# Optimization experiments

Hardware: AMD Instinct MI355X
Metric: run time of the kernel (lower is better)

Reference implementation:

```python
import jax, jax.numpy as jnp
import numpy as np

EPS = 1e-5
N_HEAD = 8

def setup_inputs() -> dict:
    key = jax.random.key(0)
    ks = jax.random.split(key, 8)
    n, c, h, w = 8, 512, 64, 64
    feats_in = 512
    x = jax.random.normal(ks[0], (n, c, h, w), jnp.float32)
    cond = jax.random.normal(ks[1], (n, feats_in), jnp.float32)
    # AdaGN linear: feats_in -> 2*c
    W_ada = jax.random.normal(ks[2], (feats_in, 2 * c), jnp.float32) * (1.0 / np.sqrt(feats_in))
    b_ada = jnp.zeros((2 * c,), jnp.float32)
    # qkv 1x1 conv: c -> 3c
    W_qkv = jax.random.normal(ks[3], (3 * c, c), jnp.float32) * (1.0 / np.sqrt(c))
    b_qkv = jnp.zeros((3 * c,), jnp.float32)
    # out 1x1 conv: c -> c
    W_out = jax.random.normal(ks[4], (c, c), jnp.float32) * (1.0 / np.sqrt(c))
    b_out = jnp.zeros((c,), jnp.float32)
    return {"x": x, "cond": cond, "W_ada": W_ada, "b_ada": b_ada,
            "W_qkv": W_qkv, "b_qkv": b_qkv, "W_out": W_out, "b_out": b_out}

def reference(x, cond, W_ada, b_ada, W_qkv, b_qkv, W_out, b_out):
    n, c, h, w = x.shape
    nh = N_HEAD
    dh = c // nh
    s = h * w
    # AdaGN: GroupNorm with 1 group, no affine, then scale/shift from cond
    scales_shifts = cond @ W_ada + b_ada  # [n, 2c]
    scales, shifts = scales_shifts[:, :c], scales_shifts[:, c:]
    xf = x.reshape(n, -1)
    mean = xf.mean(axis=1, keepdims=True)
    var = xf.var(axis=1, keepdims=True)
    normed = ((xf - mean) * jax.lax.rsqrt(var + EPS)).reshape(n, c, h, w)
    normed = shifts[:, :, None, None] + normed * (scales[:, :, None, None] + 1.0)
    # qkv 1x1 conv
    qkv = jnp.einsum('nchw,oc->nohw', normed, W_qkv) + b_qkv[None, :, None, None]
    # view [n, nh*3, dh, s] then transpose -> [n, nh*3, s, dh]
    qkv = qkv.reshape(n, nh * 3, dh, s).transpose(0, 1, 3, 2)
    q, k, v = jnp.split(qkv, 3, axis=1)  # each [n, nh, s, dh]
    scale = dh ** (-0.25)
    att = jnp.einsum('nhsd,nhtd->nhst', q * scale, k * scale)
    att = jax.nn.softmax(att, axis=-1)
    y = jnp.einsum('nhst,nhtd->nhsd', att, v)  # [n, nh, s, dh]
    y = y.transpose(0, 1, 3, 2).reshape(n, c, h, w)
    out = jnp.einsum('nchw,oc->nohw', y, W_out) + b_out[None, :, None, None]
    return x + out
```

## Files before the change

### kernel.cpp

```cpp
#include <hip/hip_runtime.h>

#define NB   8
#define CC   512
#define SS   4096
#define NHD  8
#define DH   64
#define FEAT 512
#define NPER (CC*SS)

typedef unsigned short ushort_t;
typedef __attribute__((ext_vector_type(8))) short bf16x8;
typedef __attribute__((ext_vector_type(4))) float f32x4;

__device__ inline float b2f(ushort_t h) {
    union { unsigned int u; float f; } v; v.u = ((unsigned int)h) << 16; return v.f;
}
__device__ inline ushort_t f2b(float f) {
    union { float f; unsigned int u; } v; v.f = f;
    unsigned int u = v.u;
    u += 0x7fffu + ((u >> 16) & 1u);
    return (ushort_t)(u >> 16);
}
__device__ inline void unpack8(uint4 v, ushort_t* us) {
    us[0] = v.x & 0xffff; us[1] = v.x >> 16;
    us[2] = v.y & 0xffff; us[3] = v.y >> 16;
    us[4] = v.z & 0xffff; us[5] = v.z >> 16;
    us[6] = v.w & 0xffff; us[7] = v.w >> 16;
}
__device__ inline float loadIn(const void* p, size_t idx, int isf) {
    return isf ? ((const float*)p)[idx] : b2f(((const ushort_t*)p)[idx]);
}
__device__ inline void load8(const void* p, size_t idx, int isf, float* f) {
    if (isf) {
        const float* q = (const float*)p + idx;
        float4 a = *(const float4*)q, b = *(const float4*)(q + 4);
        f[0]=a.x; f[1]=a.y; f[2]=a.z; f[3]=a.w; f[4]=b.x; f[5]=b.y; f[6]=b.z; f[7]=b.w;
    } else {
        uint4 v = *(const uint4*)((const ushort_t*)p + idx);
        ushort_t us[8]; unpack8(v, us);
        for (int j = 0; j < 8; ++j) f[j] = b2f(us[j]);
    }
}

typedef __attribute__((address_space(1))) const unsigned int gas_u32;
typedef __attribute__((address_space(3))) unsigned int las_u32;
__device__ inline void gload_lds16(const void* g, void* l) {
    __builtin_amdgcn_global_load_lds((gas_u32*)g, (las_u32*)l, 16, 0, 0);
}

__global__ void probe_kernel(const unsigned int* __restrict__ x, int* __restrict__ flag) {
    unsigned int w = x[threadIdx.x & 63];
    unsigned int elo = (w >> 7) & 0xFF;
    int hit = (elo >= 0x60 && elo <= 0x9F) ? 1 : 0;
    for (int m = 1; m < 64; m <<= 1) hit += __shfl_xor(hit, m, 64);
    if (threadIdx.x == 0) *flag = (hit >= 40) ? 0 : 1;
}

__global__ __launch_bounds__(256) void ada_kernel(
    const void* __restrict__ cond, const void* __restrict__ W,
    const void* __restrict__ bias, float* __restrict__ out,
    const int* __restrict__ flagp)
{
    int isf = *flagp;
    int n = blockIdx.x;
    int j = blockIdx.y * 256 + threadIdx.x;
    float acc = loadIn(bias, j, isf);
    for (int k = 0; k < FEAT; ++k)
        acc += loadIn(cond, (size_t)n * FEAT + k, isf) * loadIn(W, (size_t)k * (2 * CC) + j, isf);
    out[n * (2 * CC) + j] = acc;
}

__global__ __launch_bounds__(256) void stats_kernel(
    const void* __restrict__ x, float* __restrict__ part, const int* __restrict__ flagp)
{
    int isf = *flagp;
    int n = blockIdx.x, blk = blockIdx.y;
    int tid = threadIdx.x;
    float s = 0.f, ss = 0.f;
    size_t base8 = (size_t)blk * 4096 + tid;
    for (int i = 0; i < 16; ++i) {
        float f[8];
        load8(x, ((size_t)n * NPER) + (base8 + (size_t)i * 256) * 8, isf, f);
        for (int j = 0; j < 8; ++j) { s += f[j]; ss += f[j] * f[j]; }
    }
    for (int m = 1; m < 64; m <<= 1) { s += __shfl_xor(s, m, 64); ss += __shfl_xor(ss, m, 64); }
    int w = tid >> 6;
    if ((tid & 63) == 0) {
        part[(size_t)n * 512 + (blk * 4 + w) * 2 + 0] = s;
        part[(size_t)n * 512 + (blk * 4 + w) * 2 + 1] = ss;
    }
}

__global__ __launch_bounds__(256) void coef_kernel(
    const float* __restrict__ ada, const float* __restrict__ part,
    float* __restrict__ coefA, float* __restrict__ coefB)
{
    __shared__ float reds[4], redss[4], mv[2];
    int n = blockIdx.x;
    int tid = threadIdx.x;
    float s  = part[(size_t)n * 512 + tid * 2 + 0];
    float ss = part[(size_t)n * 512 + tid * 2 + 1];
    for (int m = 1; m < 64; m <<= 1) { s += __shfl_xor(s, m, 64); ss += __shfl_xor(ss, m, 64); }
    int w = tid >> 6, lane = tid & 63;
    if (lane == 0) { reds[w] = s; redss[w] = ss; }
    __syncthreads();
    if (tid == 0) {
        float S  = (reds[0] + reds[1]) + (reds[2] + reds[3]);
        float S2 = (redss[0] + redss[1]) + (redss[2] + redss[3]);
        float inv = 1.f / (float)NPER;
        float mean = S * inv;
        float var  = S2 * inv - mean * mean;
        mv[0] = mean;
        mv[1] = rsqrtf(var + 1e-5f);
    }
    __syncthreads();
    float mean = mv[0], r = mv[1];
    int c = blockIdx.y * 256 + tid;
    float a = (ada[n * (2 * CC) + c] + 1.f) * r;
    coefA[n * CC + c] = a;
    coefB[n * CC + c] = ada[n * (2 * CC) + CC + c] - mean * a;
}

__global__ __launch_bounds__(256) void wprime_kernel(
    const void* __restrict__ W, const void* __restrict__ bias,
    const float* __restrict__ coefA, const float* __restrict__ coefB,
    ushort_t* __restrict__ Wp, float* __restrict__ bias2,
    const int* __restrict__ flagp)
{
    int isf = *flagp;
    int n = blockIdx.x;
    int o = blockIdx.y * 256 + threadIdx.x;
    const float* cA = coefA + n * CC;
    const float* cB = coefB + n * CC;
    float bacc = loadIn(bias, o, isf);
    ushort_t* dst = Wp + ((size_t)n * 1536 + o) * 512;
    for (int c = 0; c < 512; c += 8) {
        float wv[8];
        load8(W, (size_t)o * 512 + c, isf, wv);
        float4 a0 = *(const float4*)&cA[c], a1 = *(const float4*)&cA[c + 4];
        float4 b0 = *(const float4*)&cB[c], b1 = *(const float4*)&cB[c + 4];
        float av[8] = {a0.x, a0.y, a0.z, a0.w, a1.x, a1.y, a1.z, a1.w};
        float bv[8] = {b0.x, b0.y, b0.z, b0.w, b1.x, b1.y, b1.z, b1.w};
        ushort_t pk[8];
        for (int j = 0; j < 8; ++j) {
            bacc += wv[j] * bv[j];
            pk[j] = f2b(wv[j] * av[j]);
        }
        *(ushort4*)&dst[c]     = make_ushort4(pk[0], pk[1], pk[2], pk[3]);
        *(ushort4*)&dst[c + 4] = make_ushort4(pk[4], pk[5], pk[6], pk[7]);
    }
    bias2[n * 1536 + o] = bacc;
}

__global__ __launch_bounds__(256) void wconv_kernel(
    const void* __restrict__ W, ushort_t* __restrict__ Wb, const int* __restrict__ flagp)
{
    int isf = *flagp;
    size_t i = ((size_t)blockIdx.x * 256 + threadIdx.x) * 8;
    float f[8];
    load8(W, i, isf, f);
    ushort_t pk[8];
    for (int j = 0; j < 8; ++j) pk[j] = f2b(f[j]);
    *(ushort4*)&Wb[i]     = make_ushort4(pk[0], pk[1], pk[2], pk[3]);
    *(ushort4*)&Wb[i + 4] = make_ushort4(pk[4], pk[5], pk[6], pk[7]);
}

__global__ __launch_bounds__(256) void xt_kernel(
    const void* __restrict__ x, ushort_t* __restrict__ xt, const int* __restrict__ flagp)
{
    __shared__ __align__(16) short xl[64][72];
    int isf = *flagp;
    int st = blockIdx.x & 63, ct = blockIdx.x >> 6;
    int n = blockIdx.y;
    int s0 = st * 64, c0 = ct * 64;
    int tid = threadIdx.x;
    for (int it = 0; it < 2; ++it) {
        int t = tid + it * 256;
        int cr = t >> 3, sc8 = t & 7;
        float f[8];
        load8(x, ((size_t)n * CC + c0 + cr) * SS + s0 + sc8 * 8, isf, f);
        ushort_t pk[8];
        for (int j = 0; j < 8; ++j) pk[j] = f2b(f[j]);
        *(ushort4*)&xl[cr][sc8 * 8]     = make_ushort4(pk[0], pk[1], pk[2], pk[3]);
        *(ushort4*)&xl[cr][sc8 * 8 + 4] = make_ushort4(pk[4], pk[5], pk[6], pk[7]);
    }
    __syncthreads();
    for (int it = 0; it < 2; ++it) {
        int t = tid + it * 256;
        int sr = t >> 3, cc8 = t & 7;
        ushort_t pk[8];
        for (int j = 0; j < 8; ++j) pk[j] = (ushort_t)xl[cc8 * 8 + j][sr];
        size_t o = ((size_t)n * SS + s0 + sr) * CC + c0 + cc8 * 8;
        *(ushort4*)&xt[o]     = make_ushort4(pk[0], pk[1], pk[2], pk[3]);
        *(ushort4*)&xt[o + 4] = make_ushort4(pk[4], pk[5], pk[6], pk[7]);
    }
}

__global__ __launch_bounds__(256) void qkv_gemm_kernel(
    const ushort_t* __restrict__ Wp, const ushort_t* __restrict__ xt,
    const float* __restrict__ bias2, ushort_t* __restrict__ C,
    int nb, int hb, int hc)
{
    __shared__ __align__(16) short Alds[3][64][64];
    __shared__ __align__(16) short Blds[64][64];
    int z = blockIdx.x;
    int nIdx = nb + z;
    int n0 = blockIdx.y * 64;
    int hh = blockIdx.z;
    int head = hb + hh;
    int hcc = hc * 64;
    int tid = threadIdx.x;
    int w = tid >> 6, lane = tid & 63;
    int quad = lane >> 4, l16 = lane & 15;
    int wm = (w >> 1) * 32, wn = (w & 1) * 32;
    const ushort_t* Ab = Wp + ((size_t)nIdx * 1536 + head * 64) * 512;
    const ushort_t* Bb = xt + ((size_t)nIdx * SS + n0) * 512;
    f32x4 acc[3][2][2] = {};

    int chunk0 = tid, chunk1 = tid + 256;
    int row0 = chunk0 >> 3, ssl0 = (chunk0 & 7) ^ (row0 & 7);
    int row1 = chunk1 >> 3, ssl1 = (chunk1 & 7) ^ (row1 & 7);
    int cb0a = w * 64, cb0b = 256 + w * 64;

    for (int k0 = 0; k0 < 512; k0 += 64) {
        __syncthreads();
        gload_lds16(&Bb[(size_t)row0 * 512 + k0 + ssl0 * 8], (short*)Blds + cb0a * 8);
        gload_lds16(&Bb[(size_t)row1 * 512 + k0 + ssl1 * 8], (short*)Blds + cb0b * 8);
        #pragma unroll
        for (int p = 0; p < 3; ++p) {
            const ushort_t* Ap = Ab + (size_t)p * 512 * 512;
            gload_lds16(&Ap[(size_t)row0 * 512 + k0 + ssl0 * 8], (short*)Alds[p] + cb0a * 8);
            gload_lds16(&Ap[(size_t)row1 * 512 + k0 + ssl1 * 8], (short*)Alds[p] + cb0b * 8);
        }
        __syncthreads();
        for (int kk = 0; kk < 2; ++kk) {
            bf16x8 bfv[2];
            for (int ni = 0; ni < 2; ++ni)
                bfv[ni] = *(const bf16x8*)&Blds[wn + ni * 16 + l16]
                                               [((kk * 4 + quad) ^ (l16 & 7)) * 8];
            #pragma unroll
            for (int p = 0; p < 3; ++p) {
                bf16x8 af[2];
                for (int mi = 0; mi < 2; ++mi)
                    af[mi] = *(const bf16x8*)&Alds[p][wm + mi * 16 + l16]
                                                     [((kk * 4 + quad) ^ (l16 & 7)) * 8];
                for (int mi = 0; mi < 2; ++mi)
                    for (int ni = 0; ni < 2; ++ni)
                        acc[p][mi][ni] = __builtin_amdgcn_mfma_f32_16x16x32_bf16(
                            af[mi], bfv[ni], acc[p][mi][ni], 0, 0, 0);
            }
        }
    }

    const float* b2p = bias2 + (size_t)nIdx * 1536;
    #pragma unroll
    for (int p = 0; p < 3; ++p) {
        int arow0 = p * 512 + head * 64;
        size_t cbase = ((size_t)(z * 3 + p) * hcc + hh * 64) * SS;
        if (p < 2) {
            const float SCL = 0.42467078f;
            for (int mi = 0; mi < 2; ++mi)
                for (int ni = 0; ni < 2; ++ni) {
                    int col = n0 + wn + ni * 16 + l16;
                    int d0 = wm + mi * 16 + quad * 4;
                    ushort_t pk[4];
                    for (int r = 0; r < 4; ++r) {
                        float v = (acc[p][mi][ni][r] + b2p[arow0 + d0 + r]) * SCL;
                        pk[r] = f2b(v);
                    }
                    *(ushort4*)&C[cbase + (size_t)col * 64 + d0] =
                        make_ushort4(pk[0], pk[1], pk[2], pk[3]);
                }
        } else {
            for (int mi = 0; mi < 2; ++mi)
                for (int ni = 0; ni < 2; ++ni) {
                    int col = n0 + wn + ni * 16 + l16;
                    for (int r = 0; r < 4; ++r) {
                        int rowl = wm + mi * 16 + quad * 4 + r;
                        float v = acc[p][mi][ni][r] + b2p[arow0 + rowl];
                        C[cbase + (size_t)rowl * SS + col] = f2b(v);
                    }
                }
        }
    }
}

__global__ __launch_bounds__(256, 4) void attn_kernel(
    const ushort_t* __restrict__ qkv,
    ushort_t* __restrict__ y,
    int nb, int hb, int hc)
{
    __shared__ __align__(16) short Klds[2][64][64];
    __shared__ __align__(16) short Vlds[2][64][64];

    int s0 = blockIdx.x * 128;
    int hl = blockIdx.y;
    int z = blockIdx.z;
    int n = nb + z;
    int hcc = hc * 64;
    const ushort_t* Q = qkv + ((size_t)(z * 3 + 0) * hcc + hl * 64) * SS;
    const ushort_t* K = qkv + ((size_t)(z * 3 + 1) * hcc + hl * 64) * SS;
    const ushort_t* V = qkv + ((size_t)(z * 3 + 2) * hcc + hl * 64) * SS;

    int tid = threadIdx.x;
    int w = tid >> 6, lane = tid & 63;
    int quad = lane >> 4, l16 = lane & 15;
    int sw = l16 & 7;

    bf16x8 qf[2][2];
    for (int si = 0; si < 2; ++si)
        for (int kk = 0; kk < 2; ++kk)
            qf[si][kk] = *(const bf16x8*)&Q[(size_t)(s0 + w * 32 + si * 16 + l16) * 64
                                            + kk * 32 + quad * 8];

    auto stage = [&](int b, int tt) {
        #pragma unroll
        for (int it = 0; it < 2; ++it) {
            int chunk = it * 256 + tid;
            int row = chunk >> 3;
            int ssl = (chunk & 7) ^ (row & 7);
            int cb0 = it * 256 + w * 64;
            gload_lds16(&K[(size_t)(tt + row) * 64 + ssl * 8], (short*)Klds[b] + cb0 * 8);
            gload_lds16(&V[(size_t)row * SS + tt + ssl * 8],   (short*)Vlds[b] + cb0 * 8);
        }
    };

    const short ONE = 0x3F80;
    bf16x8 ones = { ONE, ONE, ONE, ONE, ONE, ONE, ONE, ONE };

    f32x4 o[2][4] = {};
    f32x4 sum_acc[2] = {};

    stage(0, 0);

    for (int t0 = 0; t0 < SS; t0 += 64) {
        int cur = (t0 >> 6) & 1;
        __syncthreads();
        if (t0 + 64 < SS) stage(cur ^ 1, t0 + 64);

        for (int kk = 0; kk < 2; ++kk) {
            f32x4 sv[2][2];
            for (int ntl = 0; ntl < 2; ++ntl) {
                int nt = kk * 2 + ntl;
                bf16x8 kf0 = *(const bf16x8*)&Klds[cur][nt * 16 + l16][((0 * 4 + quad) ^ sw) * 8];
                bf16x8 kf1 = *(const bf16x8*)&Klds[cur][nt * 16 + l16][((1 * 4 + quad) ^ sw) * 8];
                for (int si = 0; si < 2; ++si) {
                    f32x4 a = { -16.f, -16.f, -16.f, -16.f };
                    a = __builtin_amdgcn_mfma_f32_16x16x32_bf16(kf0, qf[si][0], a, 0, 0, 0);
                    a = __builtin_amdgcn_mfma_f32_16x16x32_bf16(kf1, qf[si][1], a, 0, 0, 0);
                    sv[ntl][si] = a;
                }
            }

            bf16x8 vf[4];
            for (int dt = 0; dt < 4; ++dt)
                vf[dt] = *(const bf16x8*)&Vlds[cur][dt * 16 + l16][((kk * 4 + quad) ^ sw) * 8];

            for (int si = 0; si < 2; ++si) {
                float p0 = exp2f(sv[0][si][0]), p1 = exp2f(sv[0][si][1]);
                float p2 = exp2f(sv[0][si][2]), p3 = exp2f(sv[0][si][3]);
                float p4 = exp2f(sv[1][si][0]), p5 = exp2f(sv[1][si][1]);
                float p6 = exp2f(sv[1][si][2]), p7 = exp2f(sv[1][si][3]);
                unsigned int x0, x1, y0, y1;
                asm("v_cvt_pk_bf16_f32 %0, %1, %2" : "=v"(x0) : "v"(p0), "v"(p1));
                asm("v_cvt_pk_bf16_f32 %0, %1, %2" : "=v"(x1) : "v"(p2), "v"(p3));
                asm("v_cvt_pk_bf16_f32 %0, %1, %2" : "=v"(y0) : "v"(p4), "v"(p5));
                asm("v_cvt_pk_bf16_f32 %0, %1, %2" : "=v"(y1) : "v"(p6), "v"(p7));
                asm("v_permlane32_swap_b32 %0, %1" : "+v"(x0), "+v"(y0));
                asm("v_permlane32_swap_b32 %0, %1" : "+v"(x1), "+v"(y1));
                asm("v_permlane16_swap_b32 %0, %1" : "+v"(x0), "+v"(y0));
                asm("v_permlane16_swap_b32 %0, %1" : "+v"(x1), "+v"(y1));
                union { unsigned int u[4]; bf16x8 v; } frag;
                frag.u[0] = x0; frag.u[1] = x1; frag.u[2] = y0; frag.u[3] = y1;

                sum_acc[si] = __builtin_amdgcn_mfma_f32_16x16x32_bf16(frag.v, ones, sum_acc[si], 0, 0, 0);
                for (int dt = 0; dt < 4; ++dt)
                    o[si][dt] = __builtin_amdgcn_mfma_f32_16x16x32_bf16(frag.v, vf[dt], o[si][dt], 0, 0, 0);
            }
        }
    }

    for (int si = 0; si < 2; ++si) {
        f32x4 inv;
        for (int r = 0; r < 4; ++r) inv[r] = 1.0f / sum_acc[si][r];
        for (int dt = 0; dt < 4; ++dt) {
            int d = dt * 16 + l16;
            int cidx = (hb + hl) * DH + d;
            size_t bidx = ((size_t)n * CC + cidx) * SS + s0 + w * 32 + si * 16 + quad * 4;
            ushort_t pk[4];
            for (int r = 0; r < 4; ++r) pk[r] = f2b(o[si][dt][r] * inv[r]);
            *(ushort4*)&y[bidx] = make_ushort4(pk[0], pk[1], pk[2], pk[3]);
        }
    }
}

__global__ __launch_bounds__(512) void out_gemm_kernel(
    const ushort_t* __restrict__ Wb, const void* __restrict__ bias, const void* __restrict__ x,
    const ushort_t* __restrict__ ybuf, float* __restrict__ out,
    const int* __restrict__ flagp)
{
    __shared__ __align__(16) short Ylds[64][264];
    int isf = *flagp;
    int n = blockIdx.y;
    int s0 = blockIdx.x * 64;
    int tid = threadIdx.x;
    int w = tid >> 6, lane = tid & 63;
    int quad = lane >> 4, l16 = lane & 15;
    const ushort_t* Yb = ybuf + (size_t)n * ((size_t)CC * SS);
    float* Op = out + (size_t)n * NPER;

    f32x4 acc[4][4] = {};
    for (int kh = 0; kh < 2; ++kh) {
        __syncthreads();
        int ch = (tid & 255) + kh * 256;
        int cg = tid >> 8;
        for (int cb = 0; cb < 4; ++cb) {
            uint4 v = *(const uint4*)&Yb[(size_t)ch * SS + s0 + cg * 32 + cb * 8];
            ushort_t us[8]; unpack8(v, us);
            for (int j = 0; j < 8; ++j) Ylds[cg * 32 + cb * 8 + j][tid & 255] = (short)us[j];
        }
        __syncthreads();
        for (int k0 = 0; k0 < 256; k0 += 32) {
            bf16x8 af[4];
            for (int mi = 0; mi < 4; ++mi)
                af[mi] = *(const bf16x8*)&Wb[(size_t)(w * 64 + mi * 16 + l16) * 512
                                             + kh * 256 + k0 + quad * 8];
            for (int ni = 0; ni < 4; ++ni) {
                bf16x8 bfv = *(const bf16x8*)&Ylds[ni * 16 + l16][k0 + quad * 8];
                for (int mi = 0; mi < 4; ++mi)
                    acc[mi][ni] = __builtin_amdgcn_mfma_f32_16x16x32_bf16(
                        af[mi], bfv, acc[mi][ni], 0, 0, 0);
            }
        }
    }

    for (int mi = 0; mi < 4; ++mi)
        for (int ni = 0; ni < 4; ++ni) {
            int col = s0 + ni * 16 + l16;
            for (int r = 0; r < 4; ++r) {
                int m = w * 64 + mi * 16 + quad * 4 + r;
                size_t idx = (size_t)m * SS + col;
                float v = acc[mi][ni][r] + loadIn(bias, m, isf)
                        + loadIn(x, (size_t)n * NPER + idx, isf);
                Op[idx] = v;
            }
        }
}

extern "C" void kernel_launch(void* const* d_in, const int* in_sizes, int n_in,
                              void* d_out, int out_size, void* d_ws, size_t ws_size,
                              hipStream_t stream) {
    (void)in_sizes; (void)n_in; (void)out_size;
    const void* x     = d_in[0];
    const void* cond  = d_in[1];
    const void* W_ada = d_in[2];
    const void* b_ada = d_in[3];
    const void* W_qkv = d_in[4];
    const void* b_qkv = d_in[5];
    const void* W_out = d_in[6];
    const void* b_out = d_in[7];
    float* out = (float*)d_out;

    char* ws = (char*)d_ws;
    float* part   = (float*)ws;
    float* ada    = (float*)(ws + 16384);
    float* coefA  = (float*)(ws + 49152);
    float* coefB  = (float*)(ws + 65536);
    int*   flag   = (int*)(ws + 81920);
    ushort_t* woutb  = (ushort_t*)(ws + 82176);
    float* bias2  = (float*)(ws + 606464);
    ushort_t* wprime = (ushort_t*)(ws + 655616);
    ushort_t* ybuf   = (ushort_t*)(ws + 13238528);
    ushort_t* xtb    = (ushort_t*)(ws + 46792960);
    const size_t BASE = 46792960ULL + 33554432ULL;
    ushort_t* qkvbuf = (ushort_t*)(ws + BASE);

    const size_t PER_HS = (size_t)3 * 64 * SS * 2;
    size_t avail = ws_size > BASE ? ws_size - BASE : 0;
    int NC = 1, HC = 1;
    if      (avail >= 64 * PER_HS) { NC = 8; HC = 8; }
    else if (avail >= 32 * PER_HS) { NC = 4; HC = 8; }
    else if (avail >= 16 * PER_HS) { NC = 2; HC = 8; }
    else if (avail >=  8 * PER_HS) { NC = 1; HC = 8; }
    else if (avail >=  4 * PER_HS) { NC = 1; HC = 4; }
    else if (avail >=  2 * PER_HS) { NC = 1; HC = 2; }

    probe_kernel <<<1, 64, 0, stream>>>((const unsigned int*)x, flag);
    ada_kernel   <<<dim3(NB, 4),  256, 0, stream>>>(cond, W_ada, b_ada, ada, flag);
    stats_kernel <<<dim3(NB, 64), 256, 0, stream>>>(x, part, flag);
    coef_kernel  <<<dim3(NB, 2),  256, 0, stream>>>(ada, part, coefA, coefB);
    wprime_kernel<<<dim3(NB, 6),  256, 0, stream>>>(W_qkv, b_qkv, coefA, coefB, wprime, bias2, flag);
    wconv_kernel <<<dim3(128),    256, 0, stream>>>(W_out, woutb, flag);
    xt_kernel    <<<dim3(512, NB), 256, 0, stream>>>(x, xtb, flag);

    for (int nb = 0; nb < NB; nb += NC)
        for (int hb = 0; hb < NHD; hb += HC) {
            qkv_gemm_kernel<<<dim3(NC, 64, HC), 256, 0, stream>>>(
                wprime, xtb, bias2, qkvbuf, nb, hb, HC);
            attn_kernel<<<dim3(32, HC, NC), 256, 0, stream>>>(
                qkvbuf, ybuf, nb, hb, HC);
        }

    out_gemm_kernel<<<dim3(64, NB), 512, 0, stream>>>(woutb, b_out, x, ybuf, out, flag);
}
```

Measured before the change: 841.4 us.

## Store attention output token-major and read it directly in output GEMM

The attention kernel now writes its output as [n, s, c] (token-major) rather than channel-major, so the output projection GEMM can load B fragments straight from global memory with contiguous 16-byte reads. This removes the LDS transpose staging, its scalar shared-memory stores and two barriers per K half in the output GEMM. In exchange, the attention epilogue does scattered 2-byte stores with a stride of CC elements, which may hurt write coalescing. The GEMM also now relies on global/L2 reuse of Y across the 8 waves instead of shared memory.

```diff
diff --git a/kernel.cpp b/kernel.cpp
--- a/kernel.cpp
+++ b/kernel.cpp
@@ -287,7 +287,7 @@
 
 __global__ __launch_bounds__(256, 4) void attn_kernel(
     const ushort_t* __restrict__ qkv,
-    ushort_t* __restrict__ y,
+    ushort_t* __restrict__ yt,
     int nb, int hb, int hc)
 {
     __shared__ __align__(16) short Klds[2][64][64];
@@ -380,58 +380,45 @@
         }
     }
 
+    int c0 = (hb + hl) * DH;
     for (int si = 0; si < 2; ++si) {
         f32x4 inv;
         for (int r = 0; r < 4; ++r) inv[r] = 1.0f / sum_acc[si][r];
-        for (int dt = 0; dt < 4; ++dt) {
-            int d = dt * 16 + l16;
-            int cidx = (hb + hl) * DH + d;
-            size_t bidx = ((size_t)n * CC + cidx) * SS + s0 + w * 32 + si * 16 + quad * 4;
-            ushort_t pk[4];
-            for (int r = 0; r < 4; ++r) pk[r] = f2b(o[si][dt][r] * inv[r]);
-            *(ushort4*)&y[bidx] = make_ushort4(pk[0], pk[1], pk[2], pk[3]);
+        for (int r = 0; r < 4; ++r) {
+            size_t srow = (size_t)n * SS + s0 + w * 32 + si * 16 + quad * 4 + r;
+            ushort_t* yp = yt + srow * CC + c0 + l16;
+            for (int dt = 0; dt < 4; ++dt)
+                yp[dt * 16] = f2b(o[si][dt][r] * inv[r]);
         }
     }
 }
 
 __global__ __launch_bounds__(512) void out_gemm_kernel(
     const ushort_t* __restrict__ Wb, const void* __restrict__ bias, const void* __restrict__ x,
-    const ushort_t* __restrict__ ybuf, float* __restrict__ out,
+    const ushort_t* __restrict__ yt, float* __restrict__ out,
     const int* __restrict__ flagp)
 {
-    __shared__ __align__(16) short Ylds[64][264];
     int isf = *flagp;
     int n = blockIdx.y;
     int s0 = blockIdx.x * 64;
     int tid = threadIdx.x;
     int w = tid >> 6, lane = tid & 63;
     int quad = lane >> 4, l16 = lane & 15;
-    const ushort_t* Yb = ybuf + (size_t)n * ((size_t)CC * SS);
+    const ushort_t* Yt = yt + ((size_t)n * SS + s0) * CC;
     float* Op = out + (size_t)n * NPER;
 
     f32x4 acc[4][4] = {};
-    for (int kh = 0; kh < 2; ++kh) {
-        __syncthreads();
-        int ch = (tid & 255) + kh * 256;
-        int cg = tid >> 8;
-        for (int cb = 0; cb < 4; ++cb) {
-            uint4 v = *(const uint4*)&Yb[(size_t)ch * SS + s0 + cg * 32 + cb * 8];
-            ushort_t us[8]; unpack8(v, us);
-            for (int j = 0; j < 8; ++j) Ylds[cg * 32 + cb * 8 + j][tid & 255] = (short)us[j];
-        }
-        __syncthreads();
-        for (int k0 = 0; k0 < 256; k0 += 32) {
-            bf16x8 af[4];
+    for (int k0 = 0; k0 < 512; k0 += 32) {
+        bf16x8 af[4], bfv[4];
+        for (int mi = 0; mi < 4; ++mi)
+            af[mi] = *(const bf16x8*)&Wb[(size_t)(w * 64 + mi * 16 + l16) * 512
+                                         + k0 + quad * 8];
+        for (int ni = 0; ni < 4; ++ni)
+            bfv[ni] = *(const bf16x8*)&Yt[(size_t)(ni * 16 + l16) * CC + k0 + quad * 8];
+        for (int ni = 0; ni < 4; ++ni)
             for (int mi = 0; mi < 4; ++mi)
-                af[mi] = *(const bf16x8*)&Wb[(size_t)(w * 64 + mi * 16 + l16) * 512
-                                             + kh * 256 + k0 + quad * 8];
-            for (int ni = 0; ni < 4; ++ni) {
-                bf16x8 bfv = *(const bf16x8*)&Ylds[ni * 16 + l16][k0 + quad * 8];
-                for (int mi = 0; mi < 4; ++mi)
-                    acc[mi][ni] = __builtin_amdgcn_mfma_f32_16x16x32_bf16(
-                        af[mi], bfv, acc[mi][ni], 0, 0, 0);
-            }
-        }
+                acc[mi][ni] = __builtin_amdgcn_mfma_f32_16x16x32_bf16(
+                    af[mi], bfv[ni], acc[mi][ni], 0, 0, 0);
     }
 
     for (int mi = 0; mi < 4; ++mi)
```

After: 820.8 us. 2.4% less time.
